# Performance work log

Measured on AMD Instinct MI355X. Metric: run time of the kernel, lower is better.

The kernel has to match this reference:

```python
import jax, jax.numpy as jnp
import numpy as np
import math

RATIO = 16
B, C, H, W = 8, 684, 16, 64
HID, INP, AD, V, T = 256, 256, 512, 111, 36

def conv2d(x, w, b=None, padding=0):
    out = jax.lax.conv_general_dilated(x, w, (1, 1), [(padding, padding)] * 2,
                                       dimension_numbers=('NCHW', 'OIHW', 'NCHW'))
    if b is not None:
        out = out + b[None, :, None, None]
    return out

def pos_embedding_sine(mask, num_pos_feats=256, temperature=10000.0):
    # mask: [B,H,W] float. Normalized sine position embedding -> [B, 2*num_pos_feats, H, W]
    scale = 2.0 * math.pi
    eps = 1e-6
    y = jnp.cumsum(mask, axis=1)
    x = jnp.cumsum(mask, axis=2)
    y = y / (y[:, -1:, :] + eps) * scale
    x = x / (x[:, :, -1:] + eps) * scale
    i = jnp.arange(num_pos_feats, dtype=jnp.float32)
    dim_t = temperature ** (2.0 * jnp.floor(i / 2.0) / num_pos_feats)
    px = x[..., None] / dim_t  # [B,H,W,F]
    py = y[..., None] / dim_t
    def interleave(p):
        return jnp.stack((jnp.sin(p[..., 0::2]), jnp.cos(p[..., 1::2])), axis=4).reshape(p.shape[:3] + (num_pos_feats,))
    pos = jnp.concatenate((interleave(py), interleave(px)), axis=3)
    return jnp.transpose(pos, (0, 3, 1, 2))

def gru_cell(x, h, w_ih, w_hh, b_ih, b_hh):
    gi = x @ w_ih.T + b_ih
    gh = h @ w_hh.T + b_hh
    ir, iz, inn = jnp.split(gi, 3, axis=-1)
    hr, hz, hn = jnp.split(gh, 3, axis=-1)
    r = jax.nn.sigmoid(ir + hr)
    z = jax.nn.sigmoid(iz + hz)
    n = jnp.tanh(inn + r * hn)
    return (1.0 - z) * n + z * h

def setup_inputs() -> dict:
    key = jax.random.key(0)
    ks = jax.random.split(key, 32)
    s = 0.05
    d = {}
    d['cnn_features'] = jax.random.normal(ks[0], (B, C, H, W), jnp.float32)
    d['counting_preds'] = jax.random.uniform(ks[1], (B, V), jnp.float32)
    d['images_mask'] = jnp.ones((B, 1, H * RATIO, W * RATIO), jnp.float32)
    d['init_W'] = jax.random.normal(ks[2], (HID, C), jnp.float32) * s
    d['init_b'] = jax.random.normal(ks[3], (HID,), jnp.float32) * s
    d['emb'] = jax.random.normal(ks[4], (V, INP), jnp.float32) * s
    d['gru_w_ih'] = jax.random.normal(ks[5], (3 * HID, INP), jnp.float32) * s
    d['gru_w_hh'] = jax.random.normal(ks[6], (3 * HID, HID), jnp.float32) * s
    d['gru_b_ih'] = jax.random.normal(ks[7], (3 * HID,), jnp.float32) * s
    d['gru_b_hh'] = jax.random.normal(ks[8], (3 * HID,), jnp.float32) * s
    d['att_hidden_W'] = jax.random.normal(ks[9], (AD, HID), jnp.float32) * s
    d['att_hidden_b'] = jax.random.normal(ks[10], (AD,), jnp.float32) * s
    d['att_conv_w'] = jax.random.normal(ks[11], (512, 1, 11, 11), jnp.float32) * s
    d['att_weight_W'] = jax.random.normal(ks[12], (AD, 512), jnp.float32) * s
    d['alpha_convert_W'] = jax.random.normal(ks[13], (1, AD), jnp.float32) * s
    d['alpha_convert_b'] = jax.random.normal(ks[14], (1,), jnp.float32) * s
    d['enc_conv_w'] = jax.random.normal(ks[15], (AD, C, 1, 1), jnp.float32) * s
    d['enc_conv_b'] = jax.random.normal(ks[16], (AD,), jnp.float32) * s
    d['state_W'] = jax.random.normal(ks[17], (HID, HID), jnp.float32) * s
    d['state_b'] = jax.random.normal(ks[18], (HID,), jnp.float32) * s
    d['embw_W'] = jax.random.normal(ks[19], (HID, INP), jnp.float32) * s
    d['embw_b'] = jax.random.normal(ks[20], (HID,), jnp.float32) * s
    d['ctx_W'] = jax.random.normal(ks[21], (HID, C), jnp.float32) * s
    d['ctx_b'] = jax.random.normal(ks[22], (HID,), jnp.float32) * s
    d['count_W'] = jax.random.normal(ks[23], (HID, V), jnp.float32) * s
    d['count_b'] = jax.random.normal(ks[24], (HID,), jnp.float32) * s
    d['out_W'] = jax.random.normal(ks[25], (V, HID), jnp.float32) * s
    d['out_b'] = jax.random.normal(ks[26], (V,), jnp.float32) * s
    d['labels'] = jax.random.randint(ks[27], (B, T), 1, V)
    return d

def reference(cnn_features, counting_preds, images_mask, init_W, init_b, emb,
              gru_w_ih, gru_w_hh, gru_b_ih, gru_b_hh,
              att_hidden_W, att_hidden_b, att_conv_w, att_weight_W,
              alpha_convert_W, alpha_convert_b, enc_conv_w, enc_conv_b,
              state_W, state_b, embw_W, embw_b, ctx_W, ctx_b,
              count_W, count_b, out_W, out_b, labels):
    b, c, h, w = cnn_features.shape
    dmask = images_mask[:, :, ::RATIO, ::RATIO]  # [B,1,H,W]
    mask_hw = dmask[:, 0]                        # [B,H,W]
    # init hidden
    avg = jnp.sum(cnn_features * dmask, axis=(2, 3)) / jnp.sum(dmask, axis=(2, 3))
    hidden0 = jnp.tanh(avg @ init_W.T + init_b)
    counting_ctx = counting_preds @ count_W.T + count_b  # [B,HID]
    trans = conv2d(cnn_features, enc_conv_w, enc_conv_b)  # [B,AD,H,W], k=1
    trans = trans + pos_embedding_sine(mask_hw)
    trans_hw = jnp.transpose(trans, (0, 2, 3, 1))  # [B,H,W,AD]
    word0 = jnp.ones((b,), dtype=labels.dtype)
    words_in = jnp.concatenate([word0[:, None], labels[:, :-1]], axis=1)  # teacher forcing
    alpha_sum0 = jnp.zeros((b, 1, h, w), cnn_features.dtype)

    def step(carry, word):
        hidden, alpha_sum = carry
        we = emb[word]
        hidden = gru_cell(we, hidden, gru_w_ih, gru_w_hh, gru_b_ih, gru_b_hh)
        query = hidden @ att_hidden_W.T + att_hidden_b          # [B,AD]
        ast = conv2d(alpha_sum, att_conv_w, padding=5)          # [B,512,H,W]
        coverage = jnp.einsum('bchw,dc->bhwd', ast, att_weight_W)
        score = jnp.tanh(query[:, None, None, :] + coverage + trans_hw)
        energy = jnp.einsum('bhwd,d->bhw', score, alpha_convert_W[0]) + alpha_convert_b[0]
        energy = energy - energy.max()
        e = jnp.exp(energy) * mask_hw
        alpha = e / (jnp.sum(e, axis=(1, 2))[:, None, None] + 1e-10)
        alpha_sum = alpha[:, None] + alpha_sum
        ctx = jnp.einsum('bhw,bchw->bc', alpha, cnn_features)
        out_state = (hidden @ state_W.T + state_b
                     + we @ embw_W.T + embw_b
                     + ctx @ ctx_W.T + ctx_b
                     + counting_ctx)
        prob = out_state @ out_W.T + out_b
        return (hidden, alpha_sum), prob

    _, probs = jax.lax.scan(step, (hidden0, alpha_sum0), words_in.T)
    return jnp.transpose(probs, (1, 0, 2))  # [B,T,V]
```

## Files before the change

kernel.cpp:

```cpp
#include <hip/hip_runtime.h>
#include <hip/hip_bf16.h>
#include <math.h>

#define NB 8
#define NC 684
#define NH 16
#define NW 64
#define NHW 1024
#define NHID 256
#define NAD 512
#define NV 111
#define NT 36
#define KPAD 704

typedef __attribute__((ext_vector_type(8))) short bf16x8;
typedef __attribute__((ext_vector_type(4))) float f32x4;

__device__ __forceinline__ float wred_sum(float v){
  #pragma unroll
  for (int o = 32; o > 0; o >>= 1) v += __shfl_xor(v, o, 64);
  return v;
}
__device__ __forceinline__ float wred_max(float v){
  #pragma unroll
  for (int o = 32; o > 0; o >>= 1) v = fmaxf(v, __shfl_xor(v, o, 64));
  return v;
}
__device__ __forceinline__ float fsig(float x){ return 1.f/(1.f + __expf(-x)); }
__device__ __forceinline__ float ftanh(float x){ float e = __expf(2.f*x); return 1.f - 2.f/(e + 1.f); }
__device__ __forceinline__ unsigned short f2bf(float f){
  __hip_bfloat16 h = __float2bfloat16(f);
  return *(unsigned short*)&h;
}

__global__ void k_p0(const float* __restrict__ im, float* __restrict__ dmask,
                     float* __restrict__ msum, float* __restrict__ ys, float* __restrict__ xs,
                     float* __restrict__ idt, float* __restrict__ abuf)
{
  const int tid = threadIdx.x;
  for (int i = tid; i < NB*NHW; i += 256){
    int b = i >> 10, hw = i & 1023; int h = hw >> 6, w = hw & 63;
    dmask[i] = im[b*(256*1024) + (h*16)*1024 + (w*16)];
    abuf[i] = 0.f;
  }
  if (tid < 128) idt[tid] = expf(-(float)tid * (9.210340371976184f/128.f));
  __syncthreads();
  if (tid < 8){
    float s = 0.f;
    for (int i = 0; i < NHW; i++) s += dmask[tid*NHW + i];
    msum[tid] = s;
  }
  for (int p = tid; p < NB*NW; p += 256){
    int b = p >> 6, w = p & 63;
    float tot = 0.f;
    for (int h = 0; h < NH; h++) tot += dmask[b*NHW + h*64 + w];
    float inv = 6.283185307179586f/(tot + 1e-6f);
    float run = 0.f;
    for (int h = 0; h < NH; h++){ run += dmask[b*NHW + h*64 + w]; ys[b*NHW + h*64 + w] = run*inv; }
  }
  for (int p = tid; p < NB*NH; p += 256){
    int b = p >> 4, h = p & 15;
    float tot = 0.f;
    for (int w = 0; w < NW; w++) tot += dmask[b*NHW + h*64 + w];
    float inv = 6.283185307179586f/(tot + 1e-6f);
    float run = 0.f;
    for (int w = 0; w < NW; w++){ run += dmask[b*NHW + h*64 + w]; xs[b*NHW + h*64 + w] = run*inv; }
  }
}

__global__ void k_avg(const float* __restrict__ cnn, const float* __restrict__ dmask,
                      const float* __restrict__ msum, float* __restrict__ avg)
{
  int gid = blockIdx.x*blockDim.x + threadIdx.x;
  int gw = gid >> 6, lane = gid & 63;
  int nw = (gridDim.x*blockDim.x) >> 6;
  for (int ow = gw; ow < NB*NC; ow += nw){
    int b = ow / NC;
    const float* base = cnn + (size_t)ow * NHW;
    const float* dm = dmask + b*NHW;
    float s = 0.f;
    for (int i = lane; i < NHW; i += 64) s += base[i]*dm[i];
    s = wred_sum(s);
    if (lane == 0) avg[ow] = s / msum[b];
  }
}

__global__ void k_init(const float* __restrict__ avg, const float* __restrict__ iW, const float* __restrict__ ib,
                       const float* __restrict__ cp, const float* __restrict__ cW, const float* __restrict__ cb,
                       float* __restrict__ hm1, float* __restrict__ cctx)
{
  int gid = blockIdx.x*blockDim.x + threadIdx.x;
  int gw = gid >> 6, lane = gid & 63;
  int nw = (gridDim.x*blockDim.x) >> 6;
  for (int ow = gw; ow < 2*NB*NHID; ow += nw){
    if (ow < NB*NHID){
      int b = ow >> 8, j = ow & 255;
      float s = 0.f;
      for (int k = lane; k < NC; k += 64) s += avg[b*NC + k]*iW[j*NC + k];
      s = wred_sum(s);
      if (lane == 0) hm1[ow] = tanhf(s + ib[j]);
    } else {
      int o = ow - NB*NHID; int b = o >> 8, j = o & 255;
      float s = 0.f;
      for (int k = lane; k < NV; k += 64) s += cp[b*NV + k]*cW[j*NV + k];
      s = wred_sum(s);
      if (lane == 0) cctx[o] = s + cb[j];
    }
  }
}

__global__ __launch_bounds__(256) void k_cvt(const float* __restrict__ cnn, unsigned short* __restrict__ cnnT)
{
  const int hw0 = blockIdx.x << 6, c0 = blockIdx.y << 6, b = blockIdx.z;
  __shared__ float T[64][65];
  const int tid = threadIdx.x;
  #pragma unroll
  for (int u = 0; u < 16; u++){
    int idx = tid + (u<<8);
    int cc = idx >> 6, mm = idx & 63;
    int c = c0 + cc;
    T[cc][mm] = (c < NC) ? cnn[((size_t)b*NC + c)*NHW + hw0 + mm] : 0.f;
  }
  __syncthreads();
  #pragma unroll
  for (int r0 = 0; r0 < 64; r0 += 8){
    int hwl = r0 + (tid >> 5);
    int cp = (tid & 31) << 1;
    unsigned u0 = f2bf(T[cp][hwl]);
    unsigned u1 = f2bf(T[cp+1][hwl]);
    *(unsigned*)&cnnT[((size_t)((b<<10) + hw0 + hwl))*KPAD + c0 + cp] = (u1 << 16) | u0;
  }
}

__global__ void k_cvtw(const float* __restrict__ ew, unsigned short* __restrict__ ewb)
{
  int x = blockIdx.x*256 + threadIdx.x;
  if (x >= NAD*KPAD) return;
  int d = x / KPAD, c = x - d*KPAD;
  float v = (c < NC) ? ew[(size_t)d*NC + c] : 0.f;
  ewb[x] = f2bf(v);
}

__global__ __launch_bounds__(256) void k_mma_trans(const unsigned short* __restrict__ cnnT,
    const unsigned short* __restrict__ ewb, const float* __restrict__ eb,
    const float* __restrict__ ys, const float* __restrict__ xs,
    const float* __restrict__ idt, float* __restrict__ trans)
{
  const int m0 = blockIdx.x << 6;
  const int n0 = blockIdx.y << 6;
  const int b = m0 >> 10, hw0 = m0 & 1023;
  const int tid = threadIdx.x, lane = tid & 63, wv = tid >> 6;
  const int mrow = hw0 + (wv<<4) + (lane & 15);
  const int kgrp = (lane >> 4) << 3;
  const unsigned short* arow = cnnT + ((size_t)((b<<10) + mrow))*KPAD + kgrp;
  f32x4 acc[4];
  #pragma unroll
  for (int s = 0; s < 4; s++){ acc[s][0]=0.f; acc[s][1]=0.f; acc[s][2]=0.f; acc[s][3]=0.f; }
  #pragma unroll 2
  for (int k0 = 0; k0 < KPAD; k0 += 32){
    bf16x8 af = *(const bf16x8*)(arow + k0);
    #pragma unroll
    for (int s = 0; s < 4; s++){
      const unsigned short* brow = ewb + (size_t)(n0 + (s<<4) + (lane & 15))*KPAD + kgrp + k0;
      bf16x8 bf = *(const bf16x8*)brow;
      acc[s] = __builtin_amdgcn_mfma_f32_16x16x32_bf16(af, bf, acc[s], 0, 0, 0);
    }
  }
  #pragma unroll
  for (int r = 0; r < 4; r++){
    int hw = hw0 + (wv<<4) + ((lane>>4)<<2) + r;
    float ysv = ys[(b<<10)+hw], xsv = xs[(b<<10)+hw];
    #pragma unroll
    for (int s = 0; s < 4; s++){
      int d = n0 + (s<<4) + (lane & 15);
      float idtv = (d < 256) ? idt[d>>1] : idt[(d-256)>>1];
      float base = (d < 256) ? ysv : xsv;
      float arg = base*idtv;
      float pe = (d & 1) ? cosf(arg) : sinf(arg);
      trans[((size_t)((b<<10)+hw))*NAD + d] = acc[s][r] + eb[d] + pe;
    }
  }
}

__global__ __launch_bounds__(256) void k_wproj(const float* __restrict__ emb, const float* __restrict__ wih,
    const float* __restrict__ bih, const float* __restrict__ ewW, const float* __restrict__ ewb2,
    float* __restrict__ giW, float* __restrict__ embwW)
{
  const int v = blockIdx.x, g = blockIdx.y;
  const int tid = threadIdx.x;
  __shared__ float er[256];
  er[tid] = emb[(size_t)v*256 + tid];
  __syncthreads();
  if (g < 3){
    int i = (g<<8) + tid;
    float s = 0.f;
    const float* wr = wih + (size_t)i*256;
    #pragma unroll 4
    for (int k = 0; k < 256; k++) s += er[k]*wr[k];
    giW[(size_t)v*768 + i] = s + bih[i];
  } else {
    float s = 0.f;
    const float* wr = ewW + (size_t)tid*256;
    #pragma unroll 4
    for (int k = 0; k < 256; k++) s += er[k]*wr[k];
    embwW[(size_t)v*256 + tid] = s + ewb2[tid];
  }
}

__global__ __launch_bounds__(128) void k_ewo(const float* __restrict__ embwW, const float* __restrict__ oW,
                                             float* __restrict__ embwOW)
{
  const int v = blockIdx.x;
  const int u = threadIdx.x;
  __shared__ float ew[256];
  ew[u] = embwW[(size_t)v*256 + u];
  ew[128 + u] = embwW[(size_t)v*256 + 128 + u];
  __syncthreads();
  if (u < NV){
    float s = 0.f;
    const float* wr = oW + (size_t)u*256;
    #pragma unroll 4
    for (int k = 0; k < 256; k++) s += ew[k]*wr[k];
    embwOW[v*NV + u] = s;
  }
}

__global__ void k_mt(const float* __restrict__ aw, const float* __restrict__ acw, unsigned short* __restrict__ MtT)
{
  __shared__ float col[512];
  int t = blockIdx.x; int tid = threadIdx.x;
  for (int c = tid; c < 512; c += 256) col[c] = acw[(size_t)c*121 + t];
  __syncthreads();
  for (int d = tid; d < 512; d += 256){
    float s = 0.f;
    const float4* r4 = (const float4*)(aw + (size_t)d*512);
    for (int k = 0; k < 128; k++){
      float4 w = r4[k];
      s += col[k*4+0]*w.x + col[k*4+1]*w.y + col[k*4+2]*w.z + col[k*4+3]*w.w;
    }
    MtT[d*128 + t] = f2bf(s);
    if (t == 0){
      #pragma unroll
      for (int p = 121; p < 128; p++) MtT[d*128 + p] = 0;
    }
  }
}

__global__ __launch_bounds__(256) void k_so(const float* __restrict__ sW, const float* __restrict__ oW,
    const float* __restrict__ sb, const float* __restrict__ cxb, const float* __restrict__ cctx,
    const float* __restrict__ ob, float* __restrict__ SO, float* __restrict__ CB)
{
  const int v = blockIdx.x; const int tid = threadIdx.x;
  float acc = 0.f;
  for (int j = 0; j < 256; j++) acc += sW[(size_t)j*256 + tid] * oW[(size_t)v*256 + j];
  SO[(size_t)v*256 + tid] = acc;
  if (tid < 8){
    float s = ob[v];
    for (int j = 0; j < 256; j++) s += (sb[j] + cxb[j] + cctx[tid*256 + j]) * oW[(size_t)v*256 + j];
    CB[tid*NV + v] = s;
  }
}

__global__ __launch_bounds__(256) void k_co(const float* __restrict__ cxW, const float* __restrict__ oW,
                                            unsigned short* __restrict__ COb)
{
  const int c = blockIdx.x*256 + threadIdx.x;
  const int v = blockIdx.y;
  if (c >= KPAD) return;
  float acc = 0.f;
  if (v < NV && c < NC){
    for (int j = 0; j < 256; j++) acc += cxW[(size_t)j*NC + c] * oW[(size_t)v*256 + j];
  }
  COb[(size_t)v*KPAD + c] = f2bf(acc);
}

__global__ __launch_bounds__(256) void k_mma_PO(const unsigned short* __restrict__ cnnT,
    const unsigned short* __restrict__ COb, float* __restrict__ PO)
{
  const int m0 = blockIdx.x << 6;
  const int n0 = blockIdx.y << 6;
  const int b = blockIdx.z;
  const int tid = threadIdx.x, lane = tid & 63, wv = tid >> 6;
  const int mrow = m0 + (wv<<4) + (lane & 15);
  const int kgrp = (lane >> 4) << 3;
  const unsigned short* arow = cnnT + ((size_t)((b<<10) + mrow))*KPAD + kgrp;
  f32x4 acc[4];
  #pragma unroll
  for (int s = 0; s < 4; s++){ acc[s][0]=0.f; acc[s][1]=0.f; acc[s][2]=0.f; acc[s][3]=0.f; }
  #pragma unroll 2
  for (int k0 = 0; k0 < KPAD; k0 += 32){
    bf16x8 af = *(const bf16x8*)(arow + k0);
    #pragma unroll
    for (int s = 0; s < 4; s++){
      const unsigned short* brow = COb + (size_t)(n0 + (s<<4) + (lane & 15))*KPAD + kgrp + k0;
      bf16x8 bf = *(const bf16x8*)brow;
      acc[s] = __builtin_amdgcn_mfma_f32_16x16x32_bf16(af, bf, acc[s], 0, 0, 0);
    }
  }
  #pragma unroll
  for (int s = 0; s < 4; s++){
    int v = n0 + (s<<4) + (lane & 15);
    #pragma unroll
    for (int r = 0; r < 4; r++){
      int hw = m0 + (wv<<4) + ((lane>>4)<<2) + r;
      PO[(((size_t)b*128 + v)<<10) + hw] = acc[s][r];
    }
  }
}

__device__ __forceinline__ void gru_slice(const float* __restrict__ hs, const float* __restrict__ whh,
    const float* __restrict__ bhh, const float* __restrict__ gg, float* __restrict__ hdst,
    int r, int wid, int lane)
{
  #pragma unroll 1
  for (int jj = 0; jj < 8; jj++){
    int j = (r<<6) + (wid<<3) + jj;
    float sr = 0.f, sz = 0.f, sn = 0.f;
    #pragma unroll
    for (int u = 0; u < 4; u++){
      int k = lane + (u<<6);
      float hv = hs[k];
      sr += hv * whh[(size_t)j*256 + k];
      sz += hv * whh[(size_t)(j+256)*256 + k];
      sn += hv * whh[(size_t)(j+512)*256 + k];
    }
    sr = wred_sum(sr); sz = wred_sum(sz); sn = wred_sum(sn);
    if (lane == 0){
      float rr = 1.f/(1.f + expf(-(gg[j] + sr + bhh[j])));
      float zz = 1.f/(1.f + expf(-(gg[j+256] + sz + bhh[j+256])));
      float nn = tanhf(gg[j+512] + rr*(sn + bhh[j+512]));
      hdst[j] = (1.f - zz)*nn + zz*hs[j];
    }
  }
}

__global__ __launch_bounds__(512) void k_gq0(const float* __restrict__ hm1, const float* __restrict__ whh,
    const float* __restrict__ bhh, const float* __restrict__ giW, float* __restrict__ hbuf3)
{
  const int r = blockIdx.x, b = blockIdx.y;
  const int tid = threadIdx.x, lane = tid & 63, wid = tid >> 6;
  __shared__ float hs[256];
  if (tid < 256) hs[tid] = hm1[(b<<8) + tid];
  __syncthreads();
  gru_slice(hs, whh, bhh, giW + 768, hbuf3 + (b<<8), r, wid, lane);
}

__global__ void k_tr(const float* __restrict__ whh, const float* __restrict__ ahW,
                     __hip_bfloat162* __restrict__ whhTjb, __hip_bfloat162* __restrict__ ahWTb)
{
  int i = blockIdx.x*256 + threadIdx.x;
  int stride = gridDim.x*256;
  for (int x = i; x < 3*256*128; x += stride){
    int kp = x & 127, j = (x >> 7) & 255, g = x >> 15;
    float lo = whh[(size_t)((g<<8)+j)*256 + (kp<<1)];
    float hi = whh[(size_t)((g<<8)+j)*256 + (kp<<1) + 1];
    __hip_bfloat162 h2; h2.x = __float2bfloat16(lo); h2.y = __float2bfloat16(hi);
    whhTjb[x] = h2;
  }
  for (int x = i; x < 128*512; x += stride){
    int d = x & 511, kp = x >> 9;
    float lo = ahW[(size_t)d*256 + (kp<<1)];
    float hi = ahW[(size_t)d*256 + (kp<<1) + 1];
    __hip_bfloat162 h2; h2.x = __float2bfloat16(lo); h2.y = __float2bfloat16(hi);
    ahWTb[x] = h2;
  }
}

__global__ __launch_bounds__(512) void k_step(
  const float* __restrict__ dmask, const unsigned short* __restrict__ MtT,
  const float* __restrict__ trans,
  const float* __restrict__ acvW, const float* __restrict__ acvb,
  const float* __restrict__ PO, const float* __restrict__ SO,
  const float* __restrict__ CB, const float* __restrict__ embwOW,
  const float* __restrict__ giW, const int* __restrict__ lab,
  const __hip_bfloat162* __restrict__ whhTjb,
  const float* __restrict__ bhh, const __hip_bfloat162* __restrict__ ahWTb,
  const float* __restrict__ ahb, float* __restrict__ hbuf3,
  float* __restrict__ abuf, float* __restrict__ ebuf,
  float* __restrict__ out, int t)
{
  const int gid = blockIdx.x, tid = threadIdx.x;
  const int lane = tid & 63, wv = tid >> 6;
  const int b = gid >> 5, seg = gid & 31, h = seg >> 1, w0 = (seg & 1) << 5;
  __shared__ float eo[32][516];
  __shared__ float al[1024];
  __shared__ float as4[11][44];
  __shared__ unsigned short Asb[32*136];
  __shared__ float hq[256];
  __shared__ float qs[512];
  __shared__ float red[18];

  const float* eprev = ebuf + (((t+1)&1)<<13);
  float*       ecurb = ebuf + ((t&1)<<13);
  const float* aprev = abuf + (((t+1)&1)<<13);
  float*       acur  = abuf + ((t&1)<<13);

  if (t < NT && tid < 256) hq[tid] = hbuf3[(t%3)*2048 + (b<<8) + tid];

  if (t > 0){
    float e0 = eprev[(b<<10)+tid], e1 = eprev[(b<<10)+512+tid];
    float dm0 = dmask[(b<<10)+tid], dm1 = dmask[(b<<10)+512+tid];
    float m = wred_max(fmaxf(e0, e1));
    if (lane == 0) red[wv] = m;
    __syncthreads();
    if (tid == 0){
      float g = red[0];
      #pragma unroll
      for (int k = 1; k < 8; k++) g = fmaxf(g, red[k]);
      red[16] = g;
    }
    __syncthreads();
    float g = red[16];
    float x0 = __expf(e0 - g)*dm0, x1 = __expf(e1 - g)*dm1;
    float s = wred_sum(x0 + x1);
    if (lane == 0) red[wv] = s;
    __syncthreads();
    if (tid == 0){
      float ss = 0.f;
      #pragma unroll
      for (int k = 0; k < 8; k++) ss += red[k];
      red[17] = ss;
    }
    __syncthreads();
    float inv = 1.f/(red[17] + 1e-10f);
    al[tid] = x0*inv; al[512+tid] = x1*inv;
    __syncthreads();
    if (seg == 0 && t < NT){
      acur[(b<<10)+tid]     = aprev[(b<<10)+tid]     + al[tid];
      acur[(b<<10)+512+tid] = aprev[(b<<10)+512+tid] + al[512+tid];
    }
    if (wv < 4){
      int v = seg + (wv<<5);
      if (v < NV){
        int wprev = (t-1 == 0) ? 1 : lab[b*NT + t - 2];
        const float* POr = PO + (((size_t)b*128 + v)<<10);
        const float* hr = hbuf3 + ((t-1)%3)*2048 + (b<<8);
        const float* SOr = SO + (size_t)v*256;
        float a2 = 0.f;
        #pragma unroll
        for (int u = 0; u < 16; u++){ int p = lane + (u<<6); a2 += al[p]*POr[p]; }
        #pragma unroll
        for (int u = 0; u < 4; u++){ int k = lane + (u<<6); a2 += hr[k]*SOr[k]; }
        a2 = wred_sum(a2);
        if (lane == 0)
          out[((size_t)b*NT + (t-1))*NV + v] = a2 + CB[b*NV + v] + embwOW[wprev*NV + v];
      }
    }
  }
  if (t < NT){
    for (int idx = tid; idx < 11*44; idx += 512){
      int r = idx/44, c = idx - r*44;
      float v = 0.f;
      if (t > 0 && c < 42){
        int hi2 = h + r - 5, wi = w0 + c - 5;
        if ((unsigned)hi2 < 16u && (unsigned)wi < 64u){
          int p = (hi2<<6) + wi;
          v = aprev[(b<<10)+p] + al[p];
        }
      }
      as4[r][c] = v;
    }
    {
      float s2 = 0.f;
      #pragma unroll 4
      for (int kp = 0; kp < 128; kp++){
        __hip_bfloat162 w = ahWTb[(kp<<9) + tid];
        s2 += hq[kp<<1]*__bfloat162float(w.x) + hq[(kp<<1)+1]*__bfloat162float(w.y);
      }
      qs[tid] = s2 + ahb[tid];
    }
    __syncthreads();
    #pragma unroll
    for (int u = 0; u < 8; u++){
      int idx = tid + (u<<9);
      int w = idx >> 7, tap = idx & 127;
      float v = 0.f;
      if (tap < 121 && t > 0){
        int ki = tap/11, kj = tap - ki*11;
        v = as4[ki][w + kj];
      }
      Asb[w*136 + tap] = f2bf(v);
    }
    __syncthreads();
    const int mh = wv & 1, ns = wv >> 1;
    const int kg = (lane >> 4) << 3;
    f32x4 acc[8];
    #pragma unroll
    for (int s = 0; s < 8; s++){ acc[s][0]=0.f; acc[s][1]=0.f; acc[s][2]=0.f; acc[s][3]=0.f; }
    if (t > 0){
      const unsigned short* ab = &Asb[((mh<<4) + (lane & 15))*136 + kg];
      #pragma unroll
      for (int k0 = 0; k0 < 128; k0 += 32){
        bf16x8 af = *(const bf16x8*)(ab + k0);
        #pragma unroll
        for (int s = 0; s < 8; s++){
          const unsigned short* brow = MtT + (size_t)((ns<<7) + (s<<4) + (lane & 15))*128 + kg + k0;
          bf16x8 bf = *(const bf16x8*)brow;
          acc[s] = __builtin_amdgcn_mfma_f32_16x16x32_bf16(af, bf, acc[s], 0, 0, 0);
        }
      }
    }
    const float acb0 = acvb[0];
    #pragma unroll
    for (int s = 0; s < 8; s++){
      int d = (ns<<7) + (s<<4) + (lane & 15);
      float wav = acvW[d];
      float qd = qs[d];
      #pragma unroll
      for (int r = 0; r < 4; r++){
        int w = (mh<<4) + ((lane>>4)<<2) + r;
        int hw = (h<<6) + w0 + w;
        float tv = trans[((size_t)((b<<10)+hw))*NAD + d];
        eo[w][d] = wav * ftanh(qd + tv + acc[s][r]);
      }
    }
    __syncthreads();
    float* ecur = ecurb + (b<<10) + (h<<6) + w0;
    #pragma unroll
    for (int k = 0; k < 4; k++){
      int w = (wv<<2) + k;
      float sum = 0.f;
      #pragma unroll
      for (int u = 0; u < 8; u++) sum += eo[w][lane + (u<<6)];
      sum = wred_sum(sum);
      if (lane == 0) ecur[w] = sum + acb0;
    }
    if (seg < 8 && t < NT-1){
      int j = (seg<<5) + (wv<<2) + (lane>>4);
      int qg = lane & 15;
      const __hip_bfloat162* r0 = whhTjb + (size_t)j*128 + (qg<<3);
      const __hip_bfloat162* r1 = whhTjb + (size_t)(256+j)*128 + (qg<<3);
      const __hip_bfloat162* r2 = whhTjb + (size_t)(512+j)*128 + (qg<<3);
      float sr = 0.f, sz = 0.f, sn = 0.f;
      #pragma unroll
      for (int i = 0; i < 8; i++){
        int kp = (qg<<3) + i;
        float h0 = hq[kp<<1], h1 = hq[(kp<<1)+1];
        __hip_bfloat162 wr = r0[i], wz2 = r1[i], wn = r2[i];
        sr += h0*__bfloat162float(wr.x) + h1*__bfloat162float(wr.y);
        sz += h0*__bfloat162float(wz2.x) + h1*__bfloat162float(wz2.y);
        sn += h0*__bfloat162float(wn.x) + h1*__bfloat162float(wn.y);
      }
      #pragma unroll
      for (int o = 1; o < 16; o <<= 1){
        sr += __shfl_xor(sr, o, 64);
        sz += __shfl_xor(sz, o, 64);
        sn += __shfl_xor(sn, o, 64);
      }
      if (qg == 0){
        int wnext = lab[b*NT + t];
        const float* gg = giW + (size_t)wnext*768;
        float r = fsig(gg[j] + sr + bhh[j]);
        float z = fsig(gg[j+256] + sz + bhh[j+256]);
        float n = ftanh(gg[j+512] + r*(sn + bhh[j+512]));
        hbuf3[((t+1)%3)*2048 + (b<<8) + j] = (1.f - z)*n + z*hq[j];
      }
    }
  }
}

extern "C" void kernel_launch(void* const* d_in, const int* in_sizes, int n_in,
                              void* d_out, int out_size, void* d_ws, size_t ws_size,
                              hipStream_t stream)
{
  const float* cnn  = (const float*)d_in[0];
  const float* cp   = (const float*)d_in[1];
  const float* im   = (const float*)d_in[2];
  const float* iW   = (const float*)d_in[3];
  const float* ib   = (const float*)d_in[4];
  const float* emb  = (const float*)d_in[5];
  const float* wih  = (const float*)d_in[6];
  const float* whh  = (const float*)d_in[7];
  const float* bih  = (const float*)d_in[8];
  const float* bhh  = (const float*)d_in[9];
  const float* ahW  = (const float*)d_in[10];
  const float* ahb  = (const float*)d_in[11];
  const float* acw  = (const float*)d_in[12];
  const float* awW  = (const float*)d_in[13];
  const float* acvW = (const float*)d_in[14];
  const float* acvb = (const float*)d_in[15];
  const float* ecw  = (const float*)d_in[16];
  const float* ecb  = (const float*)d_in[17];
  const float* sW   = (const float*)d_in[18];
  const float* sb   = (const float*)d_in[19];
  const float* ewW  = (const float*)d_in[20];
  const float* ewb2 = (const float*)d_in[21];
  const float* cxW  = (const float*)d_in[22];
  const float* cxb  = (const float*)d_in[23];
  const float* cW   = (const float*)d_in[24];
  const float* cb   = (const float*)d_in[25];
  const float* oW   = (const float*)d_in[26];
  const float* ob   = (const float*)d_in[27];
  const int*   lab  = (const int*)d_in[28];
  float* out = (float*)d_out;
  float* ws = (float*)d_ws;

  float* dmask  = ws + 0;
  float* ys     = ws + 8192;
  float* xs     = ws + 16384;
  float* idt    = ws + 24576;
  float* msum   = ws + 24704;
  float* avg    = ws + 24720;
  float* cctx   = ws + 30192;
  float* hm1    = ws + 32240;
  float* hbuf3  = ws + 34288;
  float* abuf   = ws + 40432;
  float* ebuf   = ws + 56816;
  float* giW    = ws + 73200;
  float* embwW  = ws + 158448;
  float* embwOW = ws + 186864;
  unsigned short* MtT = (unsigned short*)(ws + 199216);
  float* SO     = ws + 231984;
  float* CB     = ws + 260400;
  __hip_bfloat162* whhTjb = (__hip_bfloat162*)(ws + 261296);
  __hip_bfloat162* ahWTb  = (__hip_bfloat162*)(ws + 359600);
  unsigned short* cnnT = (unsigned short*)(ws + 425136);
  unsigned short* ewbb = (unsigned short*)(ws + 3308720);
  unsigned short* COb  = (unsigned short*)(ws + 3488944);
  float* trans  = ws + 3534000;
  float* PO     = ws + 7728304;

  k_p0<<<1, 256, 0, stream>>>(im, dmask, msum, ys, xs, idt, abuf);
  k_avg<<<456, 256, 0, stream>>>(cnn, dmask, msum, avg);
  k_init<<<256, 256, 0, stream>>>(avg, iW, ib, cp, cW, cb, hm1, cctx);
  k_wproj<<<dim3(NV, 4), 256, 0, stream>>>(emb, wih, bih, ewW, ewb2, giW, embwW);
  k_ewo<<<NV, 128, 0, stream>>>(embwW, oW, embwOW);
  k_cvt<<<dim3(16, 11, 8), 256, 0, stream>>>(cnn, cnnT);
  k_cvtw<<<(NAD*KPAD + 255)/256, 256, 0, stream>>>(ecw, ewbb);
  k_mma_trans<<<dim3(128, 8), 256, 0, stream>>>(cnnT, ewbb, ecb, ys, xs, idt, trans);
  k_mt<<<121, 256, 0, stream>>>(awW, acw, MtT);
  k_so<<<NV, 256, 0, stream>>>(sW, oW, sb, cxb, cctx, ob, SO, CB);
  k_co<<<dim3(3, 128), 256, 0, stream>>>(cxW, oW, COb);
  k_mma_PO<<<dim3(16, 2, 8), 256, 0, stream>>>(cnnT, COb, PO);
  k_tr<<<128, 256, 0, stream>>>(whh, ahW, whhTjb, ahWTb);
  k_gq0<<<dim3(4, 8), 512, 0, stream>>>(hm1, whh, bhh, giW, hbuf3);

  for (int t = 0; t <= NT; t++){
    k_step<<<256, 512, 0, stream>>>(dmask, MtT, trans, acvW, acvb, PO, SO, CB, embwOW,
                                    giW, lab, whhTjb, bhh, ahWTb, ahb, hbuf3, abuf, ebuf, out, t);
  }
}
```

Measured before the change: 1.250 ms.

## Split step kernel across more blocks and precompute next query in GRU blocks

Each per-timestep kernel now launches 512 blocks, each handling 16 spatial positions instead of 32, so more CUs are busy on the attention energy computation. The query projection for the next step is no longer computed redundantly in every block. Instead, dedicated blocks compute the GRU update, then the next step's query, and write it to a double-buffered global qbuf. A new init kernel produces the first query. The projection GEMM also processes two M tiles per wave for more reuse of the B operand. The cost is more total blocks and extra global traffic, and correctness relies on the cross-launch ordering of the qbuf writes.

```diff
diff --git a/kernel.cpp b/kernel.cpp
--- a/kernel.cpp
+++ b/kernel.cpp
@@ -146,38 +146,45 @@
     const float* __restrict__ ys, const float* __restrict__ xs,
     const float* __restrict__ idt, float* __restrict__ trans)
 {
-  const int m0 = blockIdx.x << 6;
+  const int m0 = blockIdx.x << 7;
   const int n0 = blockIdx.y << 6;
   const int b = m0 >> 10, hw0 = m0 & 1023;
   const int tid = threadIdx.x, lane = tid & 63, wv = tid >> 6;
-  const int mrow = hw0 + (wv<<4) + (lane & 15);
   const int kgrp = (lane >> 4) << 3;
-  const unsigned short* arow = cnnT + ((size_t)((b<<10) + mrow))*KPAD + kgrp;
-  f32x4 acc[4];
-  #pragma unroll
-  for (int s = 0; s < 4; s++){ acc[s][0]=0.f; acc[s][1]=0.f; acc[s][2]=0.f; acc[s][3]=0.f; }
+  const unsigned short* arow0 = cnnT + ((size_t)((b<<10) + hw0 + (wv<<5) + (lane & 15)))*KPAD + kgrp;
+  const unsigned short* arow1 = arow0 + (size_t)16*KPAD;
+  f32x4 acc[2][4];
+  #pragma unroll
+  for (int mt=0; mt<2; mt++)
+    #pragma unroll
+    for (int s = 0; s < 4; s++){ acc[mt][s][0]=0.f; acc[mt][s][1]=0.f; acc[mt][s][2]=0.f; acc[mt][s][3]=0.f; }
   #pragma unroll 2
   for (int k0 = 0; k0 < KPAD; k0 += 32){
-    bf16x8 af = *(const bf16x8*)(arow + k0);
+    bf16x8 a0 = *(const bf16x8*)(arow0 + k0);
+    bf16x8 a1 = *(const bf16x8*)(arow1 + k0);
     #pragma unroll
     for (int s = 0; s < 4; s++){
       const unsigned short* brow = ewb + (size_t)(n0 + (s<<4) + (lane & 15))*KPAD + kgrp + k0;
       bf16x8 bf = *(const bf16x8*)brow;
-      acc[s] = __builtin_amdgcn_mfma_f32_16x16x32_bf16(af, bf, acc[s], 0, 0, 0);
-    }
-  }
-  #pragma unroll
-  for (int r = 0; r < 4; r++){
-    int hw = hw0 + (wv<<4) + ((lane>>4)<<2) + r;
-    float ysv = ys[(b<<10)+hw], xsv = xs[(b<<10)+hw];
-    #pragma unroll
-    for (int s = 0; s < 4; s++){
-      int d = n0 + (s<<4) + (lane & 15);
-      float idtv = (d < 256) ? idt[d>>1] : idt[(d-256)>>1];
-      float base = (d < 256) ? ysv : xsv;
-      float arg = base*idtv;
-      float pe = (d & 1) ? cosf(arg) : sinf(arg);
-      trans[((size_t)((b<<10)+hw))*NAD + d] = acc[s][r] + eb[d] + pe;
+      acc[0][s] = __builtin_amdgcn_mfma_f32_16x16x32_bf16(a0, bf, acc[0][s], 0, 0, 0);
+      acc[1][s] = __builtin_amdgcn_mfma_f32_16x16x32_bf16(a1, bf, acc[1][s], 0, 0, 0);
+    }
+  }
+  #pragma unroll
+  for (int mt = 0; mt < 2; mt++){
+    #pragma unroll
+    for (int r = 0; r < 4; r++){
+      int hw = hw0 + (wv<<5) + (mt<<4) + ((lane>>4)<<2) + r;
+      float ysv = ys[(b<<10)+hw], xsv = xs[(b<<10)+hw];
+      #pragma unroll
+      for (int s = 0; s < 4; s++){
+        int d = n0 + (s<<4) + (lane & 15);
+        float idtv = (d < 256) ? idt[d>>1] : idt[(d-256)>>1];
+        float base = (d < 256) ? ysv : xsv;
+        float arg = base*idtv;
+        float pe = (d & 1) ? cosf(arg) : sinf(arg);
+        trans[((size_t)((b<<10)+hw))*NAD + d] = acc[mt][s][r] + eb[d] + pe;
+      }
     }
   }
 }
@@ -345,6 +352,25 @@
   gru_slice(hs, whh, bhh, giW + 768, hbuf3 + (b<<8), r, wid, lane);
 }
 
+__global__ __launch_bounds__(512) void k_query0(const float* __restrict__ hbuf3, const float* __restrict__ ahW,
+    const float* __restrict__ ahb, float* __restrict__ qbuf)
+{
+  const int b = blockIdx.x >> 3, dc = blockIdx.x & 7;
+  const int tid = threadIdx.x, lane = tid & 63, wid = tid >> 6;
+  __shared__ float hs[256];
+  if (tid < 256) hs[tid] = hbuf3[(b<<8) + tid];
+  __syncthreads();
+  #pragma unroll 1
+  for (int i = 0; i < 8; i++){
+    int d = (dc<<6) + (wid<<3) + i;
+    float acc = 0.f;
+    #pragma unroll
+    for (int u = 0; u < 4; u++){ int k = lane + (u<<6); acc += hs[k]*ahW[(size_t)d*256 + k]; }
+    acc = wred_sum(acc);
+    if (lane == 0) qbuf[(b<<9) + d] = acc + ahb[d];
+  }
+}
+
 __global__ void k_tr(const float* __restrict__ whh, const float* __restrict__ ahW,
                      __hip_bfloat162* __restrict__ whhTjb, __hip_bfloat162* __restrict__ ahWTb)
 {
@@ -368,7 +394,7 @@
 
 __global__ __launch_bounds__(512) void k_step(
   const float* __restrict__ dmask, const unsigned short* __restrict__ MtT,
-  const float* __restrict__ trans,
+  const float* __restrict__ trans, float* __restrict__ qbuf,
   const float* __restrict__ acvW, const float* __restrict__ acvb,
   const float* __restrict__ PO, const float* __restrict__ SO,
   const float* __restrict__ CB, const float* __restrict__ embwOW,
@@ -381,21 +407,19 @@
 {
   const int gid = blockIdx.x, tid = threadIdx.x;
   const int lane = tid & 63, wv = tid >> 6;
-  const int b = gid >> 5, seg = gid & 31, h = seg >> 1, w0 = (seg & 1) << 5;
-  __shared__ float eo[32][516];
+  const int b = gid >> 6, seg = gid & 63, h = seg >> 2, w0 = (seg & 3) << 4;
+  __shared__ float eo[16][516];
   __shared__ float al[1024];
-  __shared__ float as4[11][44];
-  __shared__ unsigned short Asb[32*136];
-  __shared__ float hq[256];
+  __shared__ float as4[11][28];
+  __shared__ unsigned short Asb[16*136];
   __shared__ float qs[512];
+  __shared__ float hq[256], hn[256];
   __shared__ float red[18];
 
   const float* eprev = ebuf + (((t+1)&1)<<13);
   float*       ecurb = ebuf + ((t&1)<<13);
   const float* aprev = abuf + (((t+1)&1)<<13);
   float*       acur  = abuf + ((t&1)<<13);
-
-  if (t < NT && tid < 256) hq[tid] = hbuf3[(t%3)*2048 + (b<<8) + tid];
 
   if (t > 0){
     float e0 = eprev[(b<<10)+tid], e1 = eprev[(b<<10)+512+tid];
@@ -429,7 +453,7 @@
       acur[(b<<10)+tid]     = aprev[(b<<10)+tid]     + al[tid];
       acur[(b<<10)+512+tid] = aprev[(b<<10)+512+tid] + al[512+tid];
     }
-    if (wv < 4){
+    if (seg < 32 && wv < 4){
       int v = seg + (wv<<5);
       if (v < NV){
         int wprev = (t-1 == 0) ? 1 : lab[b*NT + t - 2];
@@ -448,10 +472,11 @@
     }
   }
   if (t < NT){
-    for (int idx = tid; idx < 11*44; idx += 512){
-      int r = idx/44, c = idx - r*44;
+    qs[tid] = qbuf[((t&1)<<12) + (b<<9) + tid];
+    for (int idx = tid; idx < 11*28; idx += 512){
+      int r = idx/28, c = idx - r*28;
       float v = 0.f;
-      if (t > 0 && c < 42){
+      if (t > 0 && c < 26){
         int hi2 = h + r - 5, wi = w0 + c - 5;
         if ((unsigned)hi2 < 16u && (unsigned)wi < 64u){
           int p = (hi2<<6) + wi;
@@ -460,18 +485,9 @@
       }
       as4[r][c] = v;
     }
-    {
-      float s2 = 0.f;
-      #pragma unroll 4
-      for (int kp = 0; kp < 128; kp++){
-        __hip_bfloat162 w = ahWTb[(kp<<9) + tid];
-        s2 += hq[kp<<1]*__bfloat162float(w.x) + hq[(kp<<1)+1]*__bfloat162float(w.y);
-      }
-      qs[tid] = s2 + ahb[tid];
-    }
-    __syncthreads();
-    #pragma unroll
-    for (int u = 0; u < 8; u++){
+    __syncthreads();
+    #pragma unroll
+    for (int u = 0; u < 4; u++){
       int idx = tid + (u<<9);
       int w = idx >> 7, tap = idx & 127;
       float v = 0.f;
@@ -482,19 +498,18 @@
       Asb[w*136 + tap] = f2bf(v);
     }
     __syncthreads();
-    const int mh = wv & 1, ns = wv >> 1;
     const int kg = (lane >> 4) << 3;
-    f32x4 acc[8];
-    #pragma unroll
-    for (int s = 0; s < 8; s++){ acc[s][0]=0.f; acc[s][1]=0.f; acc[s][2]=0.f; acc[s][3]=0.f; }
+    f32x4 acc[4];
+    #pragma unroll
+    for (int s = 0; s < 4; s++){ acc[s][0]=0.f; acc[s][1]=0.f; acc[s][2]=0.f; acc[s][3]=0.f; }
     if (t > 0){
-      const unsigned short* ab = &Asb[((mh<<4) + (lane & 15))*136 + kg];
+      const unsigned short* ab = &Asb[(lane & 15)*136 + kg];
       #pragma unroll
       for (int k0 = 0; k0 < 128; k0 += 32){
         bf16x8 af = *(const bf16x8*)(ab + k0);
         #pragma unroll
-        for (int s = 0; s < 8; s++){
-          const unsigned short* brow = MtT + (size_t)((ns<<7) + (s<<4) + (lane & 15))*128 + kg + k0;
+        for (int s = 0; s < 4; s++){
+          const unsigned short* brow = MtT + (size_t)((wv<<6) + (s<<4) + (lane & 15))*128 + kg + k0;
           bf16x8 bf = *(const bf16x8*)brow;
           acc[s] = __builtin_amdgcn_mfma_f32_16x16x32_bf16(af, bf, acc[s], 0, 0, 0);
         }
@@ -502,13 +517,13 @@
     }
     const float acb0 = acvb[0];
     #pragma unroll
-    for (int s = 0; s < 8; s++){
-      int d = (ns<<7) + (s<<4) + (lane & 15);
+    for (int s = 0; s < 4; s++){
+      int d = (wv<<6) + (s<<4) + (lane & 15);
       float wav = acvW[d];
       float qd = qs[d];
       #pragma unroll
       for (int r = 0; r < 4; r++){
-        int w = (mh<<4) + ((lane>>4)<<2) + r;
+        int w = ((lane>>4)<<2) + r;
         int hw = (h<<6) + w0 + w;
         float tv = trans[((size_t)((b<<10)+hw))*NAD + d];
         eo[w][d] = wav * ftanh(qd + tv + acc[s][r]);
@@ -517,43 +532,53 @@
     __syncthreads();
     float* ecur = ecurb + (b<<10) + (h<<6) + w0;
     #pragma unroll
-    for (int k = 0; k < 4; k++){
-      int w = (wv<<2) + k;
+    for (int k = 0; k < 2; k++){
+      int w = (wv<<1) + k;
       float sum = 0.f;
       #pragma unroll
       for (int u = 0; u < 8; u++) sum += eo[w][lane + (u<<6)];
       sum = wred_sum(sum);
       if (lane == 0) ecur[w] = sum + acb0;
     }
-    if (seg < 8 && t < NT-1){
-      int j = (seg<<5) + (wv<<2) + (lane>>4);
-      int qg = lane & 15;
-      const __hip_bfloat162* r0 = whhTjb + (size_t)j*128 + (qg<<3);
-      const __hip_bfloat162* r1 = whhTjb + (size_t)(256+j)*128 + (qg<<3);
-      const __hip_bfloat162* r2 = whhTjb + (size_t)(512+j)*128 + (qg<<3);
-      float sr = 0.f, sz = 0.f, sn = 0.f;
-      #pragma unroll
-      for (int i = 0; i < 8; i++){
-        int kp = (qg<<3) + i;
-        float h0 = hq[kp<<1], h1 = hq[(kp<<1)+1];
-        __hip_bfloat162 wr = r0[i], wz2 = r1[i], wn = r2[i];
-        sr += h0*__bfloat162float(wr.x) + h1*__bfloat162float(wr.y);
-        sz += h0*__bfloat162float(wz2.x) + h1*__bfloat162float(wz2.y);
-        sn += h0*__bfloat162float(wn.x) + h1*__bfloat162float(wn.y);
-      }
-      #pragma unroll
-      for (int o = 1; o < 16; o <<= 1){
-        sr += __shfl_xor(sr, o, 64);
-        sz += __shfl_xor(sz, o, 64);
-        sn += __shfl_xor(sn, o, 64);
-      }
-      if (qg == 0){
+    if (seg >= 32 && seg < 40 && t < NT-1){
+      if (tid < 256) hq[tid] = hbuf3[(t%3)*2048 + (b<<8) + tid];
+      __syncthreads();
+      if (tid < 256){
+        const int j = tid;
+        const __hip_bfloat162* r0 = whhTjb + (size_t)j*128;
+        const __hip_bfloat162* r1 = whhTjb + (size_t)(256+j)*128;
+        const __hip_bfloat162* r2 = whhTjb + (size_t)(512+j)*128;
+        float sr = 0.f, sz = 0.f, sn = 0.f;
+        #pragma unroll 4
+        for (int kp = 0; kp < 128; kp++){
+          float h0 = hq[kp<<1], h1 = hq[(kp<<1)+1];
+          __hip_bfloat162 wr = r0[kp], wz2 = r1[kp], wn = r2[kp];
+          sr += h0*__bfloat162float(wr.x) + h1*__bfloat162float(wr.y);
+          sz += h0*__bfloat162float(wz2.x) + h1*__bfloat162float(wz2.y);
+          sn += h0*__bfloat162float(wn.x) + h1*__bfloat162float(wn.y);
+        }
         int wnext = lab[b*NT + t];
         const float* gg = giW + (size_t)wnext*768;
         float r = fsig(gg[j] + sr + bhh[j]);
         float z = fsig(gg[j+256] + sz + bhh[j+256]);
         float n = ftanh(gg[j+512] + r*(sn + bhh[j+512]));
-        hbuf3[((t+1)%3)*2048 + (b<<8) + j] = (1.f - z)*n + z*hq[j];
+        hn[j] = (1.f - z)*n + z*hq[j];
+      }
+      __syncthreads();
+      if (seg == 32 && tid < 256) hbuf3[((t+1)%3)*2048 + (b<<8) + tid] = hn[tid];
+      {
+        int d = ((seg-32)<<6) + (tid>>3);
+        int kq = tid & 7;
+        float s2 = 0.f;
+        #pragma unroll
+        for (int i = 0; i < 16; i++){
+          int kp = (kq<<4) + i;
+          __hip_bfloat162 w = ahWTb[(kp<<9) + d];
+          s2 += hn[kp<<1]*__bfloat162float(w.x) + hn[(kp<<1)+1]*__bfloat162float(w.y);
+        }
+        #pragma unroll
+        for (int o = 1; o < 8; o <<= 1) s2 += __shfl_xor(s2, o, 64);
+        if (kq == 0) qbuf[(((t+1)&1)<<12) + (b<<9) + d] = s2 + ahb[d];
       }
     }
   }
@@ -604,21 +629,22 @@
   float* cctx   = ws + 30192;
   float* hm1    = ws + 32240;
   float* hbuf3  = ws + 34288;
-  float* abuf   = ws + 40432;
-  float* ebuf   = ws + 56816;
-  float* giW    = ws + 73200;
-  float* embwW  = ws + 158448;
-  float* embwOW = ws + 186864;
-  unsigned short* MtT = (unsigned short*)(ws + 199216);
-  float* SO     = ws + 231984;
-  float* CB     = ws + 260400;
-  __hip_bfloat162* whhTjb = (__hip_bfloat162*)(ws + 261296);
-  __hip_bfloat162* ahWTb  = (__hip_bfloat162*)(ws + 359600);
-  unsigned short* cnnT = (unsigned short*)(ws + 425136);
-  unsigned short* ewbb = (unsigned short*)(ws + 3308720);
-  unsigned short* COb  = (unsigned short*)(ws + 3488944);
-  float* trans  = ws + 3534000;
-  float* PO     = ws + 7728304;
+  float* qbuf   = ws + 40432;
+  float* abuf   = ws + 48624;
+  float* ebuf   = ws + 65008;
+  float* giW    = ws + 81392;
+  float* embwW  = ws + 166640;
+  float* embwOW = ws + 195056;
+  unsigned short* MtT = (unsigned short*)(ws + 207408);
+  float* SO     = ws + 240176;
+  float* CB     = ws + 268592;
+  __hip_bfloat162* whhTjb = (__hip_bfloat162*)(ws + 269488);
+  __hip_bfloat162* ahWTb  = (__hip_bfloat162*)(ws + 367792);
+  unsigned short* cnnT = (unsigned short*)(ws + 433328);
+  unsigned short* ewbb = (unsigned short*)(ws + 3316912);
+  unsigned short* COb  = (unsigned short*)(ws + 3497136);
+  float* trans  = ws + 3542192;
+  float* PO     = ws + 7736496;
 
   k_p0<<<1, 256, 0, stream>>>(im, dmask, msum, ys, xs, idt, abuf);
   k_avg<<<456, 256, 0, stream>>>(cnn, dmask, msum, avg);
@@ -627,16 +653,17 @@
   k_ewo<<<NV, 128, 0, stream>>>(embwW, oW, embwOW);
   k_cvt<<<dim3(16, 11, 8), 256, 0, stream>>>(cnn, cnnT);
   k_cvtw<<<(NAD*KPAD + 255)/256, 256, 0, stream>>>(ecw, ewbb);
-  k_mma_trans<<<dim3(128, 8), 256, 0, stream>>>(cnnT, ewbb, ecb, ys, xs, idt, trans);
+  k_mma_trans<<<dim3(64, 8), 256, 0, stream>>>(cnnT, ewbb, ecb, ys, xs, idt, trans);
   k_mt<<<121, 256, 0, stream>>>(awW, acw, MtT);
   k_so<<<NV, 256, 0, stream>>>(sW, oW, sb, cxb, cctx, ob, SO, CB);
   k_co<<<dim3(3, 128), 256, 0, stream>>>(cxW, oW, COb);
   k_mma_PO<<<dim3(16, 2, 8), 256, 0, stream>>>(cnnT, COb, PO);
   k_tr<<<128, 256, 0, stream>>>(whh, ahW, whhTjb, ahWTb);
   k_gq0<<<dim3(4, 8), 512, 0, stream>>>(hm1, whh, bhh, giW, hbuf3);
+  k_query0<<<64, 512, 0, stream>>>(hbuf3, ahW, ahb, qbuf);
 
   for (int t = 0; t <= NT; t++){
-    k_step<<<256, 512, 0, stream>>>(dmask, MtT, trans, acvW, acvb, PO, SO, CB, embwOW,
+    k_step<<<512, 512, 0, stream>>>(dmask, MtT, trans, qbuf, acvW, acvb, PO, SO, CB, embwOW,
                                     giW, lab, whhTjb, bhh, ahWTb, ahb, hbuf3, abuf, ebuf, out, t);
   }
 }
```

Result: slower. 1.674 ms (+33.9%).

## Store trans precomputation in bf16 and widen k_mma_trans M tile

Applied to the files above, without the earlier changes.

The precomputed trans tensor (B*HW*512) is now written as bf16 instead of fp32, which halves the bytes each of the 37 k_step launches reads from it. k_mma_trans also computes two 16-row M subtiles per wave, reusing each B fragment load, and launches half as many blocks. The cost is lower precision in the trans term that feeds the tanh energy.

```diff
diff --git a/kernel.cpp b/kernel.cpp
--- a/kernel.cpp
+++ b/kernel.cpp
@@ -31,6 +31,9 @@
 __device__ __forceinline__ unsigned short f2bf(float f){
   __hip_bfloat16 h = __float2bfloat16(f);
   return *(unsigned short*)&h;
+}
+__device__ __forceinline__ float bf2f(unsigned short u){
+  return __uint_as_float(((unsigned)u) << 16);
 }
 
 __global__ void k_p0(const float* __restrict__ im, float* __restrict__ dmask,
@@ -144,40 +147,47 @@
 __global__ __launch_bounds__(256) void k_mma_trans(const unsigned short* __restrict__ cnnT,
     const unsigned short* __restrict__ ewb, const float* __restrict__ eb,
     const float* __restrict__ ys, const float* __restrict__ xs,
-    const float* __restrict__ idt, float* __restrict__ trans)
-{
-  const int m0 = blockIdx.x << 6;
+    const float* __restrict__ idt, unsigned short* __restrict__ transb)
+{
+  const int m0 = blockIdx.x << 7;
   const int n0 = blockIdx.y << 6;
   const int b = m0 >> 10, hw0 = m0 & 1023;
   const int tid = threadIdx.x, lane = tid & 63, wv = tid >> 6;
-  const int mrow = hw0 + (wv<<4) + (lane & 15);
   const int kgrp = (lane >> 4) << 3;
-  const unsigned short* arow = cnnT + ((size_t)((b<<10) + mrow))*KPAD + kgrp;
-  f32x4 acc[4];
-  #pragma unroll
-  for (int s = 0; s < 4; s++){ acc[s][0]=0.f; acc[s][1]=0.f; acc[s][2]=0.f; acc[s][3]=0.f; }
+  const unsigned short* arow0 = cnnT + ((size_t)((b<<10) + hw0 + (wv<<5) + (lane & 15)))*KPAD + kgrp;
+  const unsigned short* arow1 = arow0 + (size_t)16*KPAD;
+  f32x4 acc[2][4];
+  #pragma unroll
+  for (int mt=0; mt<2; mt++)
+    #pragma unroll
+    for (int s = 0; s < 4; s++){ acc[mt][s][0]=0.f; acc[mt][s][1]=0.f; acc[mt][s][2]=0.f; acc[mt][s][3]=0.f; }
   #pragma unroll 2
   for (int k0 = 0; k0 < KPAD; k0 += 32){
-    bf16x8 af = *(const bf16x8*)(arow + k0);
+    bf16x8 a0 = *(const bf16x8*)(arow0 + k0);
+    bf16x8 a1 = *(const bf16x8*)(arow1 + k0);
     #pragma unroll
     for (int s = 0; s < 4; s++){
       const unsigned short* brow = ewb + (size_t)(n0 + (s<<4) + (lane & 15))*KPAD + kgrp + k0;
       bf16x8 bf = *(const bf16x8*)brow;
-      acc[s] = __builtin_amdgcn_mfma_f32_16x16x32_bf16(af, bf, acc[s], 0, 0, 0);
-    }
-  }
-  #pragma unroll
-  for (int r = 0; r < 4; r++){
-    int hw = hw0 + (wv<<4) + ((lane>>4)<<2) + r;
-    float ysv = ys[(b<<10)+hw], xsv = xs[(b<<10)+hw];
-    #pragma unroll
-    for (int s = 0; s < 4; s++){
-      int d = n0 + (s<<4) + (lane & 15);
-      float idtv = (d < 256) ? idt[d>>1] : idt[(d-256)>>1];
-      float base = (d < 256) ? ysv : xsv;
-      float arg = base*idtv;
-      float pe = (d & 1) ? cosf(arg) : sinf(arg);
-      trans[((size_t)((b<<10)+hw))*NAD + d] = acc[s][r] + eb[d] + pe;
+      acc[0][s] = __builtin_amdgcn_mfma_f32_16x16x32_bf16(a0, bf, acc[0][s], 0, 0, 0);
+      acc[1][s] = __builtin_amdgcn_mfma_f32_16x16x32_bf16(a1, bf, acc[1][s], 0, 0, 0);
+    }
+  }
+  #pragma unroll
+  for (int mt = 0; mt < 2; mt++){
+    #pragma unroll
+    for (int r = 0; r < 4; r++){
+      int hw = hw0 + (wv<<5) + (mt<<4) + ((lane>>4)<<2) + r;
+      float ysv = ys[(b<<10)+hw], xsv = xs[(b<<10)+hw];
+      #pragma unroll
+      for (int s = 0; s < 4; s++){
+        int d = n0 + (s<<4) + (lane & 15);
+        float idtv = (d < 256) ? idt[d>>1] : idt[(d-256)>>1];
+        float base = (d < 256) ? ysv : xsv;
+        float arg = base*idtv;
+        float pe = (d & 1) ? cosf(arg) : sinf(arg);
+        transb[((size_t)((b<<10)+hw))*NAD + d] = f2bf(acc[mt][s][r] + eb[d] + pe);
+      }
     }
   }
 }
@@ -368,7 +378,7 @@
 
 __global__ __launch_bounds__(512) void k_step(
   const float* __restrict__ dmask, const unsigned short* __restrict__ MtT,
-  const float* __restrict__ trans,
+  const unsigned short* __restrict__ transb,
   const float* __restrict__ acvW, const float* __restrict__ acvb,
   const float* __restrict__ PO, const float* __restrict__ SO,
   const float* __restrict__ CB, const float* __restrict__ embwOW,
@@ -510,7 +520,7 @@
       for (int r = 0; r < 4; r++){
         int w = (mh<<4) + ((lane>>4)<<2) + r;
         int hw = (h<<6) + w0 + w;
-        float tv = trans[((size_t)((b<<10)+hw))*NAD + d];
+        float tv = bf2f(transb[((size_t)((b<<10)+hw))*NAD + d]);
         eo[w][d] = wav * ftanh(qd + tv + acc[s][r]);
       }
     }
@@ -617,8 +627,8 @@
   unsigned short* cnnT = (unsigned short*)(ws + 425136);
   unsigned short* ewbb = (unsigned short*)(ws + 3308720);
   unsigned short* COb  = (unsigned short*)(ws + 3488944);
-  float* trans  = ws + 3534000;
-  float* PO     = ws + 7728304;
+  unsigned short* transb = (unsigned short*)(ws + 3534000);
+  float* PO     = ws + 5631152;
 
   k_p0<<<1, 256, 0, stream>>>(im, dmask, msum, ys, xs, idt, abuf);
   k_avg<<<456, 256, 0, stream>>>(cnn, dmask, msum, avg);
@@ -627,7 +637,7 @@
   k_ewo<<<NV, 128, 0, stream>>>(embwW, oW, embwOW);
   k_cvt<<<dim3(16, 11, 8), 256, 0, stream>>>(cnn, cnnT);
   k_cvtw<<<(NAD*KPAD + 255)/256, 256, 0, stream>>>(ecw, ewbb);
-  k_mma_trans<<<dim3(128, 8), 256, 0, stream>>>(cnnT, ewbb, ecb, ys, xs, idt, trans);
+  k_mma_trans<<<dim3(64, 8), 256, 0, stream>>>(cnnT, ewbb, ecb, ys, xs, idt, transb);
   k_mt<<<121, 256, 0, stream>>>(awW, acw, MtT);
   k_so<<<NV, 256, 0, stream>>>(sW, oW, sb, cxb, cctx, ob, SO, CB);
   k_co<<<dim3(3, 128), 256, 0, stream>>>(cxW, oW, COb);
@@ -636,7 +646,7 @@
   k_gq0<<<dim3(4, 8), 512, 0, stream>>>(hm1, whh, bhh, giW, hbuf3);
 
   for (int t = 0; t <= NT; t++){
-    k_step<<<256, 512, 0, stream>>>(dmask, MtT, trans, acvW, acvb, PO, SO, CB, embwOW,
+    k_step<<<256, 512, 0, stream>>>(dmask, MtT, transb, acvW, acvb, PO, SO, CB, embwOW,
                                     giW, lab, whhTjb, bhh, ahWTb, ahb, hbuf3, abuf, ebuf, out, t);
   }
 }
```

New measurement: 1.068 ms. 14.6% less time.
